# Optimization experiments

Measured on AMD Instinct MI355X. Metric: run time of the kernel, lower is better.

The kernel has to match this reference:

```python
import jax, jax.numpy as jnp
import numpy as np

K, B, S, D, V, H = 4, 64, 50, 256, 40000, 4
DH = D // H
TOPK = 2
NEG = -1e9
SCALE = float(1.0 / np.sqrt(DH))


def setup_inputs() -> dict:
    key = jax.random.key(0)
    ks = jax.random.split(key, 16)
    s = 0.05
    return {
        "ids":   jax.random.randint(ks[0], (K, B, S), 0, V),
        "items": jax.random.randint(ks[1], (K, B, S), 0, V),
        "adj":   jax.random.randint(ks[2], (B, S, S), 0, 5),
        "alias": jax.random.randint(ks[3], (B, S), 0, S),
        "eps":   jax.random.normal(ks[4], (B, S, K), jnp.float32),
        "emb":   jax.random.normal(ks[5], (K, V, D), jnp.float32) * s,
        "agg_a": jax.random.normal(ks[6], (K, 4, D), jnp.float32) * s,
        "Wq": jax.random.normal(ks[7], (K, D, D), jnp.float32) * s,
        "Wk": jax.random.normal(ks[8], (K, D, D), jnp.float32) * s,
        "Wv": jax.random.normal(ks[9], (K, D, D), jnp.float32) * s,
        "Wo": jax.random.normal(ks[10], (K, D, D), jnp.float32) * s,
        "ln1_g": jnp.ones((K, D), jnp.float32),
        "ln1_b": jnp.zeros((K, D), jnp.float32),
        "W1": jax.random.normal(ks[11], (K, D, 4 * D), jnp.float32) * s,
        "W2": jax.random.normal(ks[12], (K, 4 * D, D), jnp.float32) * s,
        "ln2_g": jnp.ones((K, D), jnp.float32),
        "ln2_b": jnp.zeros((K, D), jnp.float32),
        "Wg": jax.random.normal(ks[13], (D, K), jnp.float32) * s,
        "Wn": jax.random.normal(ks[14], (D, K), jnp.float32) * s,
    }


def _layer_norm(x, g, b):
    m = jnp.mean(x, -1, keepdims=True)
    v = jnp.var(x, -1, keepdims=True)
    return (x - m) * jax.lax.rsqrt(v + 1e-5) * g + b


def _per_key(ids, items, emb, a, Wq, Wk, Wv, Wo, g1, b1, W1, W2, g2, b2, adj, alias):
    hg = emb[items]                                          # [B,S,D] graph-node embeddings
    # LocalAggregator: relation-typed pairwise attention over session graph (adj in {1..4})
    e = jnp.einsum('bid,bjd,rd->rbij', hg, hg, a)            # [4,B,S,S], avoids [B,S,S,D]
    e = jax.nn.leaky_relu(e, 0.2)
    alpha = jnp.full(adj.shape, NEG, e.dtype)
    for r in range(4):
        alpha = jnp.where(adj == r + 1, e[r], alpha)
    alpha = jax.nn.softmax(alpha, -1)
    h_local = jnp.einsum('bij,bjd->bid', alpha, hg)          # graph aggregation
    h = jnp.take_along_axis(h_local, alias[..., None], axis=1)   # distribute graph rows to sequence
    # memory-transformer block (pre-LN causal MHA + FFN)
    x = _layer_norm(h, g1, b1)
    q = (x @ Wq).reshape(B, S, H, DH)
    k = (x @ Wk).reshape(B, S, H, DH)
    v = (x @ Wv).reshape(B, S, H, DH)
    scores = jnp.einsum('bihd,bjhd->bhij', q, k) * SCALE
    causal = jnp.tril(jnp.ones((S, S), bool))
    scores = jnp.where(causal, scores, NEG)
    attn = jax.nn.softmax(scores, -1)
    o = jnp.einsum('bhij,bjhd->bihd', attn, v).reshape(B, S, D) @ Wo
    h = h + o
    y = _layer_norm(h, g2, b2)
    h = h + jax.nn.gelu(y @ W1) @ W2
    return h


def reference(ids, items, adj, alias, eps, emb, agg_a, Wq, Wk, Wv, Wo,
              ln1_g, ln1_b, W1, W2, ln2_g, ln2_b, Wg, Wn):
    per_key = jax.vmap(_per_key, in_axes=(0,) * 14 + (None, None))
    h_keys = per_key(ids, items, emb, agg_a, Wq, Wk, Wv, Wo,
                     ln1_g, ln1_b, W1, W2, ln2_g, ln2_b, adj, alias)   # [K,B,S,D]
    # gate input: mean over per-key input-sequence embeddings (h_seq in original)
    h_seq = jax.vmap(lambda e, i: e[i])(emb, ids).mean(0)              # [B,S,D]
    # noisy top-k gating over node-type experts
    logits = h_seq @ Wg + jax.nn.softplus(h_seq @ Wn) * eps            # [B,S,K]
    top_v, top_i = jax.lax.top_k(logits, TOPK)
    w = jax.nn.softmax(top_v, -1)                                      # [B,S,TOPK]
    gates = jnp.sum(jax.nn.one_hot(top_i, K, dtype=w.dtype) * w[..., None], axis=-2)  # [B,S,K]
    return jnp.einsum('bsk,kbsd->bsd', gates, h_keys)
```

## Files before the change

kernel.cpp:

```cpp
#include <hip/hip_runtime.h>
#include <hip/hip_bf16.h>
#include <math.h>

#define K_ 4
#define B_ 64
#define S_ 50
#define D_ 256
#define V_ 40000
#define H_ 4
#define DH_ 64
#define NEG_ (-1e9f)
#define SCALE_ 0.125f

typedef __attribute__((ext_vector_type(8))) __bf16 bf16x8v;
typedef __attribute__((ext_vector_type(4))) float f32x4v;

__device__ __forceinline__ float wred_sum(float v) {
#pragma unroll
  for (int off = 32; off > 0; off >>= 1) v += __shfl_xor(v, off, 64);
  return v;
}
__device__ __forceinline__ float wred_max(float v) {
#pragma unroll
  for (int off = 32; off > 0; off >>= 1) v = fmaxf(v, __shfl_xor(v, off, 64));
  return v;
}
__device__ __forceinline__ float softplusf(float x) {
  return (x > 20.f) ? x : log1pf(expf(x));
}
__device__ __forceinline__ float geluf(float x) {
  const float c = 0.7978845608028654f;
  float x3 = x * x * x;
  return 0.5f * x * (1.f + tanhf(c * (x + 0.044715f * x3)));
}
__device__ __forceinline__ float bf2f(unsigned int u) {
  return __uint_as_float(u << 16);
}
__device__ __forceinline__ unsigned short f2bf(float f) {
  unsigned u = __float_as_uint(f);
  return (unsigned short)((u + 0x7fffu + ((u >> 16) & 1u)) >> 16);
}
__device__ __forceinline__ void unp8(uint4 a, float* d) {
  d[0] = bf2f(a.x & 0xffffu); d[1] = bf2f(a.x >> 16);
  d[2] = bf2f(a.y & 0xffffu); d[3] = bf2f(a.y >> 16);
  d[4] = bf2f(a.z & 0xffffu); d[5] = bf2f(a.z >> 16);
  d[6] = bf2f(a.w & 0xffffu); d[7] = bf2f(a.w >> 16);
}
__device__ __forceinline__ bf16x8v cvt8(float4 a, float4 b) {
  bf16x8v r;
  r[0] = (__bf16)a.x; r[1] = (__bf16)a.y; r[2] = (__bf16)a.z; r[3] = (__bf16)a.w;
  r[4] = (__bf16)b.x; r[5] = (__bf16)b.y; r[6] = (__bf16)b.z; r[7] = (__bf16)b.w;
  return r;
}

__global__ __launch_bounds__(256) void front_kernel(
    const int* __restrict__ items, const int* __restrict__ adj,
    const float* __restrict__ emb, const float* __restrict__ agg_a,
    float* __restrict__ h_raw,
    const int* __restrict__ ids, const float* __restrict__ Wg,
    const float* __restrict__ Wn, const float* __restrict__ eps,
    float* __restrict__ gates,
    const float* __restrict__ wq, const float* __restrict__ wk,
    const float* __restrict__ wv, const float* __restrict__ wo,
    const float* __restrict__ w1, const float* __restrict__ w2,
    unsigned short* __restrict__ wqkvT, unsigned short* __restrict__ woT,
    unsigned short* __restrict__ w1T, unsigned short* __restrict__ w2T) {
  __shared__ __bf16 hgb[64][264];
  __shared__ float e_f[50][68];
  __shared__ __bf16 alp[64][72];
  __shared__ unsigned char adj_s[64][64];
  __shared__ __bf16 a_sb[4][264];
  int bid = blockIdx.x;
  int t = threadIdx.x;

  if (bid < 256) {
    int kb = bid;
    int k = kb >> 6, b = kb & 63;
    for (int c = t; c < 2048; c += 256) {
      int row = c >> 5, c8 = (c & 31) * 8;
      bf16x8v val;
      if (row < S_) {
        int g = items[kb * S_ + row];
        const float* src = emb + ((long)k * V_ + g) * D_ + c8;
        val = cvt8(*(const float4*)src, *(const float4*)(src + 4));
      } else {
#pragma unroll
        for (int e = 0; e < 8; ++e) val[e] = (__bf16)0.f;
      }
      *(bf16x8v*)&hgb[row][c8] = val;
    }
    if (t < 128) {
      int row = t >> 5, c8 = (t & 31) * 8;
      const float* src = agg_a + ((long)k * 4 + row) * D_ + c8;
      *(bf16x8v*)&a_sb[row][c8] = cvt8(*(const float4*)src, *(const float4*)(src + 4));
    }
    for (int c = t; c < 4096; c += 256) {
      int i = c >> 6, j = c & 63;
      adj_s[i][j] = (i < S_ && j < S_)
                        ? (unsigned char)adj[((long)b * S_ + i) * S_ + j] : 0;
    }
    __syncthreads();
    int w = t >> 6, lane = t & 63;
    int m16 = lane & 15, quad = lane >> 4;
    float e_sel[4][4];
#pragma unroll
    for (int nt = 0; nt < 4; ++nt)
#pragma unroll
      for (int rg = 0; rg < 4; ++rg) e_sel[nt][rg] = NEG_;
#pragma unroll
    for (int r = 0; r < 4; ++r) {
      f32x4v acc[4];
#pragma unroll
      for (int nt = 0; nt < 4; ++nt) acc[nt] = (f32x4v){0.f, 0.f, 0.f, 0.f};
#pragma unroll
      for (int k0 = 0; k0 < 8; ++k0) {
        int kc = k0 * 32 + quad * 8;
        bf16x8v hr = *(const bf16x8v*)&hgb[w * 16 + m16][kc];
        bf16x8v ar = *(const bf16x8v*)&a_sb[r][kc];
        bf16x8v af;
#pragma unroll
        for (int e = 0; e < 8; ++e) af[e] = (__bf16)((float)hr[e] * (float)ar[e]);
#pragma unroll
        for (int nt = 0; nt < 4; ++nt) {
          bf16x8v bf = *(const bf16x8v*)&hgb[nt * 16 + m16][kc];
          acc[nt] = __builtin_amdgcn_mfma_f32_16x16x32_bf16(af, bf, acc[nt], 0, 0, 0);
        }
      }
#pragma unroll
      for (int nt = 0; nt < 4; ++nt)
#pragma unroll
        for (int rg = 0; rg < 4; ++rg) {
          int i = w * 16 + quad * 4 + rg, j = nt * 16 + m16;
          if (adj_s[i][j] == r + 1) {
            float v = acc[nt][rg];
            e_sel[nt][rg] = (v >= 0.f) ? v : 0.2f * v;
          }
        }
    }
#pragma unroll
    for (int nt = 0; nt < 4; ++nt)
#pragma unroll
      for (int rg = 0; rg < 4; ++rg) {
        int i = w * 16 + quad * 4 + rg;
        if (i < S_) e_f[i][nt * 16 + m16] = e_sel[nt][rg];
      }
    __syncthreads();
    for (int i = w; i < S_; i += 4) {
      float val = (lane < S_) ? e_f[i][lane] : -INFINITY;
      float m = wred_max(val);
      float p = expf(val - m);
      float ssum = wred_sum(p);
      alp[i][lane] = (__bf16)(p / ssum);
    }
    __syncthreads();
#pragma unroll 4
    for (int nt = 0; nt < 16; ++nt) {
      f32x4v acc = (f32x4v){0.f, 0.f, 0.f, 0.f};
#pragma unroll
      for (int k0 = 0; k0 < 2; ++k0) {
        int jb = k0 * 32 + quad * 8;
        bf16x8v af = *(const bf16x8v*)&alp[w * 16 + m16][jb];
        bf16x8v bf;
#pragma unroll
        for (int tt = 0; tt < 8; ++tt) bf[tt] = hgb[jb + tt][nt * 16 + m16];
        acc = __builtin_amdgcn_mfma_f32_16x16x32_bf16(af, bf, acc, 0, 0, 0);
      }
#pragma unroll
      for (int rg = 0; rg < 4; ++rg) {
        int i = w * 16 + quad * 4 + rg;
        if (i < S_)
          h_raw[((long)kb * S_ + i) * D_ + nt * 16 + m16] = acc[rg];
      }
    }
    return;
  }

  if (bid < 1024) {
    int tid = bid - 256;
    typedef unsigned short row66[66];
    row66* tile = (row66*)&hgb[0][0];
    const float* src; unsigned short* dst; int C, R; int r0, c0;
    if (tid < 192) {
      int sect = tid >> 6; int rem = tid & 63;
      int k = rem >> 4, t2 = rem & 15;
      r0 = (t2 >> 2) * 64; c0 = (t2 & 3) * 64;
      src = ((sect == 0) ? wq : (sect == 1) ? wk : wv) + (long)k * 65536;
      dst = wqkvT + ((long)k * 768 + sect * 256) * 256;
      R = 256; C = 256;
    } else if (tid < 256) {
      int rem = tid - 192; int k = rem >> 4, t2 = rem & 15;
      r0 = (t2 >> 2) * 64; c0 = (t2 & 3) * 64;
      src = wo + (long)k * 65536; dst = woT + (long)k * 65536;
      R = 256; C = 256;
    } else if (tid < 512) {
      int rem = tid - 256; int k = rem >> 6, t2 = rem & 63;
      r0 = (t2 >> 4) * 64; c0 = (t2 & 15) * 64;
      src = w1 + (long)k * 262144; dst = w1T + (long)k * 262144;
      R = 256; C = 1024;
    } else {
      int rem = tid - 512; int k = rem >> 6, t2 = rem & 63;
      r0 = (t2 >> 2) * 64; c0 = (t2 & 3) * 64;
      src = w2 + (long)k * 262144; dst = w2T + (long)k * 262144;
      R = 1024; C = 256;
    }
    int sr = t >> 2, sc = (t & 3) * 16;
    const float* p = src + (long)(r0 + sr) * C + c0 + sc;
#pragma unroll
    for (int q = 0; q < 4; ++q) {
      float4 f = *(const float4*)(p + q * 4);
      tile[sr][sc + q * 4 + 0] = f2bf(f.x);
      tile[sr][sc + q * 4 + 1] = f2bf(f.y);
      tile[sr][sc + q * 4 + 2] = f2bf(f.z);
      tile[sr][sc + q * 4 + 3] = f2bf(f.w);
    }
    __syncthreads();
    int dc = t >> 2, ch = (t & 3) * 16;
    unsigned int wds[8];
#pragma unroll
    for (int i = 0; i < 8; ++i)
      wds[i] = (unsigned int)tile[ch + 2 * i][dc] |
               ((unsigned int)tile[ch + 2 * i + 1][dc] << 16);
    unsigned short* dp = dst + (long)(c0 + dc) * R + r0 + ch;
    uint4 o0 = make_uint4(wds[0], wds[1], wds[2], wds[3]);
    uint4 o1 = make_uint4(wds[4], wds[5], wds[6], wds[7]);
    *(uint4*)dp = o0;
    *(uint4*)(dp + 8) = o1;
    return;
  }

  {
    int w = t >> 6, lane = t & 63;
    int item = (bid - 1024) * 4 + w;
    int b = item / S_, s = item % S_;
    int d0 = lane * 4;
    float4 hs = make_float4(0.f, 0.f, 0.f, 0.f);
#pragma unroll
    for (int k = 0; k < K_; ++k) {
      int id = ids[(k * B_ + b) * S_ + s];
      const float4 e = *(const float4*)(emb + ((long)k * V_ + id) * D_ + d0);
      hs.x += e.x; hs.y += e.y; hs.z += e.z; hs.w += e.w;
    }
    hs.x *= 0.25f; hs.y *= 0.25f; hs.z *= 0.25f; hs.w *= 0.25f;
    float logit[4];
#pragma unroll
    for (int j = 0; j < K_; ++j) {
      float pg = hs.x * Wg[(d0 + 0) * K_ + j] + hs.y * Wg[(d0 + 1) * K_ + j] +
                 hs.z * Wg[(d0 + 2) * K_ + j] + hs.w * Wg[(d0 + 3) * K_ + j];
      float pn = hs.x * Wn[(d0 + 0) * K_ + j] + hs.y * Wn[(d0 + 1) * K_ + j] +
                 hs.z * Wn[(d0 + 2) * K_ + j] + hs.w * Wn[(d0 + 3) * K_ + j];
      pg = wred_sum(pg);
      pn = wred_sum(pn);
      logit[j] = pg + softplusf(pn) * eps[item * K_ + j];
    }
    if (lane == 0) {
      int i0 = 0; float v0 = logit[0];
      for (int j = 1; j < K_; ++j) if (logit[j] > v0) { v0 = logit[j]; i0 = j; }
      int i1 = -1; float v1 = 0.f;
      for (int j = 0; j < K_; ++j)
        if (j != i0 && (i1 < 0 || logit[j] > v1)) { v1 = logit[j]; i1 = j; }
      float w0 = 1.f / (1.f + expf(v1 - v0));
      float w1 = 1.f - w0;
#pragma unroll
      for (int j = 0; j < K_; ++j)
        gates[item * K_ + j] = (j == i0) ? w0 : ((j == i1) ? w1 : 0.f);
    }
  }
}

__global__ __launch_bounds__(256) void gather_ln(
    const float* __restrict__ h_raw, const int* __restrict__ alias_,
    float* __restrict__ hbuf, unsigned short* __restrict__ xb,
    const float* __restrict__ g, const float* __restrict__ bta) {
  int kb = blockIdx.x;
  int k = kb >> 6, b = kb & 63;
  int w = threadIdx.x >> 6, lane = threadIdx.x & 63;
  for (int s = w; s < S_; s += 4) {
    int src = alias_[b * S_ + s];
    const float4 v = *(const float4*)(h_raw + ((long)kb * S_ + src) * D_ + lane * 4);
    long off = ((long)kb * S_ + s) * D_ + lane * 4;
    *(float4*)(hbuf + off) = v;
    float sum = wred_sum(v.x + v.y + v.z + v.w);
    float sq = wred_sum(v.x * v.x + v.y * v.y + v.z * v.z + v.w * v.w);
    float mean = sum * (1.f / D_);
    float var = sq * (1.f / D_) - mean * mean;
    float rs = rsqrtf(var + 1e-5f);
    const float4 gv = *(const float4*)(g + k * D_ + lane * 4);
    const float4 bv = *(const float4*)(bta + k * D_ + lane * 4);
    ushort4 o;
    o.x = f2bf((v.x - mean) * rs * gv.x + bv.x);
    o.y = f2bf((v.y - mean) * rs * gv.y + bv.y);
    o.z = f2bf((v.z - mean) * rs * gv.z + bv.z);
    o.w = f2bf((v.w - mean) * rs * gv.w + bv.w);
    *(ushort4*)(xb + off) = o;
  }
}

__global__ __launch_bounds__(256) void bgemm2(
    const unsigned short* __restrict__ A, const unsigned short* __restrict__ Bt,
    long strideA, long strideBt, int N, int Kd,
    float* __restrict__ Cf, long strideCf,
    const float* __restrict__ R, long strideR,
    unsigned short* __restrict__ Cb, long strideCb, int act) {
  __shared__ unsigned short sA[64][72];
  __shared__ unsigned short sB[64][72];
  int z = blockIdx.z;
  A += (long)z * strideA;
  Bt += (long)z * strideBt;
  int t = threadIdx.x, w = t >> 6, lane = t & 63;
  int row0 = blockIdx.y * 64, col0 = blockIdx.x * 64;
  int m16 = lane & 15, quad = lane >> 4;
  f32x4v acc[4];
#pragma unroll
  for (int nt = 0; nt < 4; ++nt) acc[nt] = (f32x4v){0.f, 0.f, 0.f, 0.f};
  int sr = t >> 2, sc = (t & 3) * 16;
  const unsigned short* pa = A + (long)(row0 + sr) * Kd + sc;
  const unsigned short* pb = Bt + (long)(col0 + sr) * Kd + sc;
  uint4 a0 = *(const uint4*)(pa);
  uint4 a1 = *(const uint4*)(pa + 8);
  uint4 b0 = *(const uint4*)(pb);
  uint4 b1 = *(const uint4*)(pb + 8);
  for (int k0 = 0; k0 < Kd; k0 += 64) {
    __syncthreads();
    *(uint4*)&sA[sr][sc] = a0;
    *(uint4*)&sA[sr][sc + 8] = a1;
    *(uint4*)&sB[sr][sc] = b0;
    *(uint4*)&sB[sr][sc + 8] = b1;
    if (k0 + 64 < Kd) {
      a0 = *(const uint4*)(pa + k0 + 64);
      a1 = *(const uint4*)(pa + k0 + 72);
      b0 = *(const uint4*)(pb + k0 + 64);
      b1 = *(const uint4*)(pb + k0 + 72);
    }
    __syncthreads();
#pragma unroll
    for (int half = 0; half < 2; ++half) {
      int kg = half * 32 + quad * 8;
      bf16x8v af = *(const bf16x8v*)&sA[w * 16 + m16][kg];
#pragma unroll
      for (int nt = 0; nt < 4; ++nt) {
        bf16x8v bf = *(const bf16x8v*)&sB[nt * 16 + m16][kg];
        acc[nt] = __builtin_amdgcn_mfma_f32_16x16x32_bf16(af, bf, acc[nt], 0, 0, 0);
      }
    }
  }
  int rbase = row0 + w * 16 + quad * 4;
  int cb = m16;
#pragma unroll
  for (int nt = 0; nt < 4; ++nt) {
#pragma unroll
    for (int i2 = 0; i2 < 4; ++i2) {
      long off = (long)(rbase + i2) * N + col0 + nt * 16 + cb;
      float vv = acc[nt][i2];
      if (R) vv += R[(long)z * strideR + off];
      if (act == 1) vv = geluf(vv);
      if (Cf) Cf[(long)z * strideCf + off] = vv;
      if (Cb) Cb[(long)z * strideCb + off] = f2bf(vv);
    }
  }
}

__global__ __launch_bounds__(256) void attn_kernel(
    const unsigned short* __restrict__ qkv, unsigned short* __restrict__ o) {
  __shared__ float qs[S_][65], ks[S_][65], vs[S_][65];
  int idx = blockIdx.x;
  int h = idx & 3;
  int kb = idx >> 2;
  long base = (long)kb * S_ * 768;
  int t = threadIdx.x;
  for (int f = t; f < S_ * 8; f += 256) {
    int row = f >> 3, c8 = (f & 7) * 8;
    long g = base + (long)row * 768 + h * DH_ + c8;
    unp8(*(const uint4*)(qkv + g), &qs[row][c8]);
    unp8(*(const uint4*)(qkv + g + 256), &ks[row][c8]);
    unp8(*(const uint4*)(qkv + g + 512), &vs[row][c8]);
  }
  __syncthreads();
  int w = t >> 6, lane = t & 63;
  for (int i = w; i < S_; i += 4) {
    int jj = (lane < S_) ? lane : 0;
    float dot = 0.f;
#pragma unroll
    for (int d = 0; d < DH_; ++d) dot = fmaf(qs[i][d], ks[jj][d], dot);
    float val = (lane <= i) ? dot * SCALE_ : ((lane < S_) ? NEG_ : -INFINITY);
    float m = wred_max(val);
    float p = expf(val - m);
    float ssum = wred_sum(p);
    float pr = p / ssum;
    float acc = 0.f;
    for (int j = 0; j <= i; ++j)
      acc = fmaf(__shfl(pr, j, 64), vs[j][lane], acc);
    o[((long)kb * S_ + i) * D_ + h * DH_ + lane] = f2bf(acc);
  }
}

__global__ __launch_bounds__(256) void bgemm_oln(
    const unsigned short* __restrict__ A, const unsigned short* __restrict__ Bt,
    float* __restrict__ hbuf, unsigned short* __restrict__ y,
    const float* __restrict__ g2, const float* __restrict__ b2) {
  __shared__ unsigned short sA[64][72];
  __shared__ unsigned short sB[256][72];
  const long BSD = (long)B_ * S_ * D_;
  int z = blockIdx.z;
  const unsigned short* Ap = A + (long)z * BSD;
  const unsigned short* Bp = Bt + (long)z * 65536;
  int t = threadIdx.x, w = t >> 6, lane = t & 63;
  int row0 = blockIdx.x * 64;
  int m16 = lane & 15, quad = lane >> 4;
  f32x4v acc[16];
#pragma unroll
  for (int nt = 0; nt < 16; ++nt) acc[nt] = (f32x4v){0.f, 0.f, 0.f, 0.f};
  int sr = t >> 2, sc = (t & 3) * 16;
  const unsigned short* pa = Ap + (long)(row0 + sr) * 256 + sc;
  const unsigned short* pb = Bp + (long)sr * 256 + sc;
  uint4 a0 = *(const uint4*)pa;
  uint4 a1 = *(const uint4*)(pa + 8);
  uint4 bv[8];
#pragma unroll
  for (int q = 0; q < 4; ++q) {
    bv[2 * q] = *(const uint4*)(pb + q * 16384);
    bv[2 * q + 1] = *(const uint4*)(pb + q * 16384 + 8);
  }
  for (int k0 = 0; k0 < 256; k0 += 64) {
    __syncthreads();
    *(uint4*)&sA[sr][sc] = a0;
    *(uint4*)&sA[sr][sc + 8] = a1;
#pragma unroll
    for (int q = 0; q < 4; ++q) {
      *(uint4*)&sB[q * 64 + sr][sc] = bv[2 * q];
      *(uint4*)&sB[q * 64 + sr][sc + 8] = bv[2 * q + 1];
    }
    if (k0 + 64 < 256) {
      a0 = *(const uint4*)(pa + k0 + 64);
      a1 = *(const uint4*)(pa + k0 + 72);
#pragma unroll
      for (int q = 0; q < 4; ++q) {
        bv[2 * q] = *(const uint4*)(pb + q * 16384 + k0 + 64);
        bv[2 * q + 1] = *(const uint4*)(pb + q * 16384 + k0 + 72);
      }
    }
    __syncthreads();
#pragma unroll
    for (int half = 0; half < 2; ++half) {
      int kg = half * 32 + quad * 8;
      bf16x8v af = *(const bf16x8v*)&sA[w * 16 + m16][kg];
#pragma unroll
      for (int nt = 0; nt < 16; ++nt) {
        bf16x8v bf = *(const bf16x8v*)&sB[nt * 16 + m16][kg];
        acc[nt] = __builtin_amdgcn_mfma_f32_16x16x32_bf16(af, bf, acc[nt], 0, 0, 0);
      }
    }
  }
  long zoff = (long)z * BSD;
  int rbase = row0 + w * 16 + quad * 4;
#pragma unroll
  for (int nt = 0; nt < 16; ++nt)
#pragma unroll
    for (int i2 = 0; i2 < 4; ++i2) {
      long off = zoff + (long)(rbase + i2) * 256 + nt * 16 + m16;
      float vv = acc[nt][i2] + hbuf[off];
      acc[nt][i2] = vv;
      hbuf[off] = vv;
    }
  float mean[4], rstd[4];
#pragma unroll
  for (int i2 = 0; i2 < 4; ++i2) {
    float s = 0.f, q = 0.f;
#pragma unroll
    for (int nt = 0; nt < 16; ++nt) {
      float vv = acc[nt][i2];
      s += vv; q += vv * vv;
    }
#pragma unroll
    for (int off = 1; off < 16; off <<= 1) {
      s += __shfl_xor(s, off, 64);
      q += __shfl_xor(q, off, 64);
    }
    float m = s * (1.f / D_);
    float var = q * (1.f / D_) - m * m;
    mean[i2] = m;
    rstd[i2] = rsqrtf(var + 1e-5f);
  }
#pragma unroll
  for (int nt = 0; nt < 16; ++nt) {
    float gv = g2[z * D_ + nt * 16 + m16];
    float bvv = b2[z * D_ + nt * 16 + m16];
#pragma unroll
    for (int i2 = 0; i2 < 4; ++i2) {
      long off = zoff + (long)(rbase + i2) * 256 + nt * 16 + m16;
      y[off] = f2bf((acc[nt][i2] - mean[i2]) * rstd[i2] * gv + bvv);
    }
  }
}

__global__ __launch_bounds__(256) void bgemm_f2a(
    const unsigned short* __restrict__ A, const unsigned short* __restrict__ Bt,
    const float* __restrict__ hbuf, const float* __restrict__ gates,
    float* __restrict__ out) {
  __shared__ unsigned short sA[64][72];
  __shared__ unsigned short sB[64][72];
  const long T4 = 3276800;
  const long BSD = (long)B_ * S_ * D_;
  int z = blockIdx.z;
  int t = threadIdx.x, w = t >> 6, lane = t & 63;
  int col0 = blockIdx.x * 64, row0 = blockIdx.y * 64;
  int m16 = lane & 15, quad = lane >> 4;
  f32x4v acc[4];
#pragma unroll
  for (int nt = 0; nt < 4; ++nt) acc[nt] = (f32x4v){0.f, 0.f, 0.f, 0.f};
  int sr = t >> 2, sc = (t & 3) * 16;
  const unsigned short* pa = A + (long)z * T4 + (long)(row0 + sr) * 1024 + sc;
  const unsigned short* pb = Bt + (long)z * 262144 + (long)(col0 + sr) * 1024 + sc;
  uint4 a0 = *(const uint4*)pa;
  uint4 a1 = *(const uint4*)(pa + 8);
  uint4 b0 = *(const uint4*)pb;
  uint4 b1 = *(const uint4*)(pb + 8);
  for (int k0 = 0; k0 < 1024; k0 += 64) {
    __syncthreads();
    *(uint4*)&sA[sr][sc] = a0;
    *(uint4*)&sA[sr][sc + 8] = a1;
    *(uint4*)&sB[sr][sc] = b0;
    *(uint4*)&sB[sr][sc + 8] = b1;
    if (k0 + 64 < 1024) {
      a0 = *(const uint4*)(pa + k0 + 64);
      a1 = *(const uint4*)(pa + k0 + 72);
      b0 = *(const uint4*)(pb + k0 + 64);
      b1 = *(const uint4*)(pb + k0 + 72);
    }
    __syncthreads();
#pragma unroll
    for (int half = 0; half < 2; ++half) {
      int kg = half * 32 + quad * 8;
      bf16x8v af = *(const bf16x8v*)&sA[w * 16 + m16][kg];
#pragma unroll
      for (int nt = 0; nt < 4; ++nt) {
        bf16x8v bf = *(const bf16x8v*)&sB[nt * 16 + m16][kg];
        acc[nt] = __builtin_amdgcn_mfma_f32_16x16x32_bf16(af, bf, acc[nt], 0, 0, 0);
      }
    }
  }
  int rbase = row0 + w * 16 + quad * 4;
#pragma unroll
  for (int i2 = 0; i2 < 4; ++i2) {
    float gz = gates[(rbase + i2) * 4 + z];
    if (gz != 0.f) {
#pragma unroll
      for (int nt = 0; nt < 4; ++nt) {
        long off = (long)(rbase + i2) * 256 + col0 + nt * 16 + m16;
        float vv = gz * (acc[nt][i2] + hbuf[(long)z * BSD + off]);
        atomicAdd(&out[off], vv);
      }
    }
  }
}

extern "C" void kernel_launch(void* const* d_in, const int* in_sizes, int n_in,
                              void* d_out, int out_size, void* d_ws,
                              size_t ws_size, hipStream_t stream) {
  const int* ids = (const int*)d_in[0];
  const int* items = (const int*)d_in[1];
  const int* adj = (const int*)d_in[2];
  const int* alias = (const int*)d_in[3];
  const float* eps = (const float*)d_in[4];
  const float* emb = (const float*)d_in[5];
  const float* agg_a = (const float*)d_in[6];
  const float* Wq = (const float*)d_in[7];
  const float* Wk = (const float*)d_in[8];
  const float* Wv = (const float*)d_in[9];
  const float* Wo = (const float*)d_in[10];
  const float* ln1g = (const float*)d_in[11];
  const float* ln1b = (const float*)d_in[12];
  const float* W1 = (const float*)d_in[13];
  const float* W2 = (const float*)d_in[14];
  const float* ln2g = (const float*)d_in[15];
  const float* ln2b = (const float*)d_in[16];
  const float* Wg = (const float*)d_in[17];
  const float* Wn = (const float*)d_in[18];
  float* out = (float*)d_out;

  const long BSD = (long)B_ * S_ * D_;
  float* ws = (float*)d_ws;
  float* gates = ws;
  float* hbuf = ws + 16384;
  unsigned short* ub = (unsigned short*)(ws + 16384 + 4 * BSD);
  unsigned short* xb = ub;
  unsigned short* qkvb = ub + 3276800;
  unsigned short* tb = qkvb;
  float* h_raw = (float*)qkvb;
  unsigned short* wqkvT = ub + 16384000;
  unsigned short* woT = wqkvT + 786432;
  unsigned short* w1T = woT + 262144;
  unsigned short* w2T = w1T + 1048576;

  const long T4 = 3276800;

  hipMemsetAsync(out, 0, (size_t)BSD * sizeof(float), stream);

  front_kernel<<<1824, 256, 0, stream>>>(
      items, adj, emb, agg_a, h_raw, ids, Wg, Wn, eps, gates,
      Wq, Wk, Wv, Wo, W1, W2, wqkvT, woT, w1T, w2T);
  gather_ln<<<256, 256, 0, stream>>>(h_raw, alias, hbuf, xb, ln1g, ln1b);
  bgemm2<<<dim3(12, 50, 4), 256, 0, stream>>>(xb, wqkvT, BSD, 196608, 768, 256,
      (float*)0, 0, (const float*)0, 0, qkvb, 2457600, 0);
  attn_kernel<<<K_ * B_ * H_, 256, 0, stream>>>(qkvb, xb);
  bgemm_oln<<<dim3(50, 1, 4), 256, 0, stream>>>(xb, woT, hbuf, xb, ln2g, ln2b);
  bgemm2<<<dim3(16, 50, 4), 256, 0, stream>>>(xb, w1T, BSD, 262144, 1024, 256,
      (float*)0, 0, (const float*)0, 0, tb, T4, 1);
  bgemm_f2a<<<dim3(4, 50, 4), 256, 0, stream>>>(tb, w2T, hbuf, gates, out);
}
```

Measured before the change: 425.9 us.

## Fuse alias gather and LayerNorm into front kernel; use 128x128 GEMM tiles

```diff
diff --git a/kernel.cpp b/kernel.cpp
--- a/kernel.cpp
+++ b/kernel.cpp
@@ -56,7 +56,9 @@
 __global__ __launch_bounds__(256) void front_kernel(
     const int* __restrict__ items, const int* __restrict__ adj,
     const float* __restrict__ emb, const float* __restrict__ agg_a,
-    float* __restrict__ h_raw,
+    const int* __restrict__ alias_, float* __restrict__ hbuf,
+    unsigned short* __restrict__ xb,
+    const float* __restrict__ ln1g, const float* __restrict__ ln1b,
     const int* __restrict__ ids, const float* __restrict__ Wg,
     const float* __restrict__ Wn, const float* __restrict__ eps,
     float* __restrict__ gates,
@@ -65,15 +67,19 @@
     const float* __restrict__ w1, const float* __restrict__ w2,
     unsigned short* __restrict__ wqkvT, unsigned short* __restrict__ woT,
     unsigned short* __restrict__ w1T, unsigned short* __restrict__ w2T) {
-  __shared__ __bf16 hgb[64][264];
-  __shared__ float e_f[50][68];
-  __shared__ __bf16 alp[64][72];
-  __shared__ unsigned char adj_s[64][64];
-  __shared__ __bf16 a_sb[4][264];
+  __shared__ __align__(16) char smem[62816];
   int bid = blockIdx.x;
   int t = threadIdx.x;
 
   if (bid < 256) {
+    typedef __bf16 (*arr264)[264];
+    arr264 hgb = (arr264)smem;
+    float (*e_f)[68] = (float(*)[68])(smem + 33792);
+    unsigned char (*adj_s)[64] = (unsigned char(*)[64])(smem + 47392);
+    arr264 a_sb = (arr264)(smem + 51488);
+    __bf16 (*alp)[72] = (__bf16(*)[72])(smem + 53600);
+    float* hl = (float*)smem;
+
     int kb = bid;
     int k = kb >> 6, b = kb & 63;
     for (int c = t; c < 2048; c += 256) {
@@ -153,7 +159,8 @@
       alp[i][lane] = (__bf16)(p / ssum);
     }
     __syncthreads();
-#pragma unroll 4
+    f32x4v acc16[16];
+#pragma unroll
     for (int nt = 0; nt < 16; ++nt) {
       f32x4v acc = (f32x4v){0.f, 0.f, 0.f, 0.f};
 #pragma unroll
@@ -165,12 +172,35 @@
         for (int tt = 0; tt < 8; ++tt) bf[tt] = hgb[jb + tt][nt * 16 + m16];
         acc = __builtin_amdgcn_mfma_f32_16x16x32_bf16(af, bf, acc, 0, 0, 0);
       }
+      acc16[nt] = acc;
+    }
+    __syncthreads();
+#pragma unroll
+    for (int nt = 0; nt < 16; ++nt)
 #pragma unroll
       for (int rg = 0; rg < 4; ++rg) {
         int i = w * 16 + quad * 4 + rg;
-        if (i < S_)
-          h_raw[((long)kb * S_ + i) * D_ + nt * 16 + m16] = acc[rg];
-      }
+        if (i < S_) hl[i * 260 + nt * 16 + m16] = acc16[nt][rg];
+      }
+    __syncthreads();
+    for (int s = w; s < S_; s += 4) {
+      int src = alias_[b * S_ + s];
+      const float4 v = *(const float4*)&hl[src * 260 + lane * 4];
+      long off = ((long)kb * S_ + s) * D_ + lane * 4;
+      *(float4*)(hbuf + off) = v;
+      float sum = wred_sum(v.x + v.y + v.z + v.w);
+      float sq = wred_sum(v.x * v.x + v.y * v.y + v.z * v.z + v.w * v.w);
+      float mean = sum * (1.f / D_);
+      float var = sq * (1.f / D_) - mean * mean;
+      float rs = rsqrtf(var + 1e-5f);
+      const float4 gv = *(const float4*)(ln1g + k * D_ + lane * 4);
+      const float4 bv = *(const float4*)(ln1b + k * D_ + lane * 4);
+      ushort4 o;
+      o.x = f2bf((v.x - mean) * rs * gv.x + bv.x);
+      o.y = f2bf((v.y - mean) * rs * gv.y + bv.y);
+      o.z = f2bf((v.z - mean) * rs * gv.z + bv.z);
+      o.w = f2bf((v.w - mean) * rs * gv.w + bv.w);
+      *(ushort4*)(xb + off) = o;
     }
     return;
   }
@@ -178,7 +208,7 @@
   if (bid < 1024) {
     int tid = bid - 256;
     typedef unsigned short row66[66];
-    row66* tile = (row66*)&hgb[0][0];
+    row66* tile = (row66*)smem;
     const float* src; unsigned short* dst; int C, R; int r0, c0;
     if (tid < 192) {
       int sect = tid >> 6; int rem = tid & 63;
@@ -267,94 +297,85 @@
   }
 }
 
-__global__ __launch_bounds__(256) void gather_ln(
-    const float* __restrict__ h_raw, const int* __restrict__ alias_,
-    float* __restrict__ hbuf, unsigned short* __restrict__ xb,
-    const float* __restrict__ g, const float* __restrict__ bta) {
-  int kb = blockIdx.x;
-  int k = kb >> 6, b = kb & 63;
-  int w = threadIdx.x >> 6, lane = threadIdx.x & 63;
-  for (int s = w; s < S_; s += 4) {
-    int src = alias_[b * S_ + s];
-    const float4 v = *(const float4*)(h_raw + ((long)kb * S_ + src) * D_ + lane * 4);
-    long off = ((long)kb * S_ + s) * D_ + lane * 4;
-    *(float4*)(hbuf + off) = v;
-    float sum = wred_sum(v.x + v.y + v.z + v.w);
-    float sq = wred_sum(v.x * v.x + v.y * v.y + v.z * v.z + v.w * v.w);
-    float mean = sum * (1.f / D_);
-    float var = sq * (1.f / D_) - mean * mean;
-    float rs = rsqrtf(var + 1e-5f);
-    const float4 gv = *(const float4*)(g + k * D_ + lane * 4);
-    const float4 bv = *(const float4*)(bta + k * D_ + lane * 4);
-    ushort4 o;
-    o.x = f2bf((v.x - mean) * rs * gv.x + bv.x);
-    o.y = f2bf((v.y - mean) * rs * gv.y + bv.y);
-    o.z = f2bf((v.z - mean) * rs * gv.z + bv.z);
-    o.w = f2bf((v.w - mean) * rs * gv.w + bv.w);
-    *(ushort4*)(xb + off) = o;
-  }
-}
-
-__global__ __launch_bounds__(256) void bgemm2(
+__global__ __launch_bounds__(256) void bgemm3(
     const unsigned short* __restrict__ A, const unsigned short* __restrict__ Bt,
     long strideA, long strideBt, int N, int Kd,
-    float* __restrict__ Cf, long strideCf,
-    const float* __restrict__ R, long strideR,
     unsigned short* __restrict__ Cb, long strideCb, int act) {
-  __shared__ unsigned short sA[64][72];
-  __shared__ unsigned short sB[64][72];
+  __shared__ unsigned short sA[128][72];
+  __shared__ unsigned short sB[128][72];
   int z = blockIdx.z;
   A += (long)z * strideA;
   Bt += (long)z * strideBt;
   int t = threadIdx.x, w = t >> 6, lane = t & 63;
-  int row0 = blockIdx.y * 64, col0 = blockIdx.x * 64;
+  int wr = w >> 1, wc = w & 1;
+  int row0 = blockIdx.y * 128, col0 = blockIdx.x * 128;
   int m16 = lane & 15, quad = lane >> 4;
-  f32x4v acc[4];
-#pragma unroll
-  for (int nt = 0; nt < 4; ++nt) acc[nt] = (f32x4v){0.f, 0.f, 0.f, 0.f};
-  int sr = t >> 2, sc = (t & 3) * 16;
+  f32x4v acc[4][4];
+#pragma unroll
+  for (int mr = 0; mr < 4; ++mr)
+#pragma unroll
+    for (int nr = 0; nr < 4; ++nr) acc[mr][nr] = (f32x4v){0.f, 0.f, 0.f, 0.f};
+  int sr = t >> 1, sc = (t & 1) * 32;
   const unsigned short* pa = A + (long)(row0 + sr) * Kd + sc;
   const unsigned short* pb = Bt + (long)(col0 + sr) * Kd + sc;
   uint4 a0 = *(const uint4*)(pa);
   uint4 a1 = *(const uint4*)(pa + 8);
+  uint4 a2 = *(const uint4*)(pa + 16);
+  uint4 a3 = *(const uint4*)(pa + 24);
   uint4 b0 = *(const uint4*)(pb);
   uint4 b1 = *(const uint4*)(pb + 8);
+  uint4 b2 = *(const uint4*)(pb + 16);
+  uint4 b3 = *(const uint4*)(pb + 24);
   for (int k0 = 0; k0 < Kd; k0 += 64) {
     __syncthreads();
     *(uint4*)&sA[sr][sc] = a0;
     *(uint4*)&sA[sr][sc + 8] = a1;
+    *(uint4*)&sA[sr][sc + 16] = a2;
+    *(uint4*)&sA[sr][sc + 24] = a3;
     *(uint4*)&sB[sr][sc] = b0;
     *(uint4*)&sB[sr][sc + 8] = b1;
+    *(uint4*)&sB[sr][sc + 16] = b2;
+    *(uint4*)&sB[sr][sc + 24] = b3;
     if (k0 + 64 < Kd) {
       a0 = *(const uint4*)(pa + k0 + 64);
       a1 = *(const uint4*)(pa + k0 + 72);
+      a2 = *(const uint4*)(pa + k0 + 80);
+      a3 = *(const uint4*)(pa + k0 + 88);
       b0 = *(const uint4*)(pb + k0 + 64);
       b1 = *(const uint4*)(pb + k0 + 72);
+      b2 = *(const uint4*)(pb + k0 + 80);
+      b3 = *(const uint4*)(pb + k0 + 88);
     }
     __syncthreads();
 #pragma unroll
     for (int half = 0; half < 2; ++half) {
       int kg = half * 32 + quad * 8;
-      bf16x8v af = *(const bf16x8v*)&sA[w * 16 + m16][kg];
-#pragma unroll
-      for (int nt = 0; nt < 4; ++nt) {
-        bf16x8v bf = *(const bf16x8v*)&sB[nt * 16 + m16][kg];
-        acc[nt] = __builtin_amdgcn_mfma_f32_16x16x32_bf16(af, bf, acc[nt], 0, 0, 0);
-      }
-    }
-  }
-  int rbase = row0 + w * 16 + quad * 4;
-  int cb = m16;
-#pragma unroll
-  for (int nt = 0; nt < 4; ++nt) {
-#pragma unroll
-    for (int i2 = 0; i2 < 4; ++i2) {
-      long off = (long)(rbase + i2) * N + col0 + nt * 16 + cb;
-      float vv = acc[nt][i2];
-      if (R) vv += R[(long)z * strideR + off];
-      if (act == 1) vv = geluf(vv);
-      if (Cf) Cf[(long)z * strideCf + off] = vv;
-      if (Cb) Cb[(long)z * strideCb + off] = f2bf(vv);
+      bf16x8v af[4], bf[4];
+#pragma unroll
+      for (int i = 0; i < 4; ++i) {
+        af[i] = *(const bf16x8v*)&sA[wr * 64 + i * 16 + m16][kg];
+        bf[i] = *(const bf16x8v*)&sB[wc * 64 + i * 16 + m16][kg];
+      }
+#pragma unroll
+      for (int mr = 0; mr < 4; ++mr)
+#pragma unroll
+        for (int nr = 0; nr < 4; ++nr)
+          acc[mr][nr] = __builtin_amdgcn_mfma_f32_16x16x32_bf16(
+              af[mr], bf[nr], acc[mr][nr], 0, 0, 0);
+    }
+  }
+#pragma unroll
+  for (int mr = 0; mr < 4; ++mr) {
+    int rbase = row0 + wr * 64 + mr * 16 + quad * 4;
+#pragma unroll
+    for (int nr = 0; nr < 4; ++nr) {
+      int col = col0 + wc * 64 + nr * 16 + m16;
+#pragma unroll
+      for (int i2 = 0; i2 < 4; ++i2) {
+        float vv = acc[mr][nr][i2];
+        if (act == 1) vv = geluf(vv);
+        Cb[(long)z * strideCb + (long)(rbase + i2) * N + col] = f2bf(vv);
+      }
     }
   }
 }
@@ -585,7 +606,6 @@
   unsigned short* xb = ub;
   unsigned short* qkvb = ub + 3276800;
   unsigned short* tb = qkvb;
-  float* h_raw = (float*)qkvb;
   unsigned short* wqkvT = ub + 16384000;
   unsigned short* woT = wqkvT + 786432;
   unsigned short* w1T = woT + 262144;
@@ -596,14 +616,14 @@
   hipMemsetAsync(out, 0, (size_t)BSD * sizeof(float), stream);
 
   front_kernel<<<1824, 256, 0, stream>>>(
-      items, adj, emb, agg_a, h_raw, ids, Wg, Wn, eps, gates,
+      items, adj, emb, agg_a, alias, hbuf, xb, ln1g, ln1b,
+      ids, Wg, Wn, eps, gates,
       Wq, Wk, Wv, Wo, W1, W2, wqkvT, woT, w1T, w2T);
-  gather_ln<<<256, 256, 0, stream>>>(h_raw, alias, hbuf, xb, ln1g, ln1b);
-  bgemm2<<<dim3(12, 50, 4), 256, 0, stream>>>(xb, wqkvT, BSD, 196608, 768, 256,
-      (float*)0, 0, (const float*)0, 0, qkvb, 2457600, 0);
+  bgemm3<<<dim3(6, 25, 4), 256, 0, stream>>>(xb, wqkvT, BSD, 196608, 768, 256,
+      qkvb, 2457600, 0);
   attn_kernel<<<K_ * B_ * H_, 256, 0, stream>>>(qkvb, xb);
   bgemm_oln<<<dim3(50, 1, 4), 256, 0, stream>>>(xb, woT, hbuf, xb, ln2g, ln2b);
-  bgemm2<<<dim3(16, 50, 4), 256, 0, stream>>>(xb, w1T, BSD, 262144, 1024, 256,
-      (float*)0, 0, (const float*)0, 0, tb, T4, 1);
+  bgemm3<<<dim3(8, 25, 4), 256, 0, stream>>>(xb, w1T, BSD, 262144, 1024, 256,
+      tb, T4, 1);
   bgemm_f2a<<<dim3(4, 50, 4), 256, 0, stream>>>(tb, w2T, hbuf, gates, out);
 }
```

New measurement: 429.5 us. No clear change (+0.9%).
